# Kernel optimization log

Measured on AMD Instinct MI355X. Metric: run time of the kernel, lower is better.

Reference implementation:

```python
import jax, jax.numpy as jnp
import numpy as np

N_NODES = 100000
N_EDGES = 1600000
IN_CH = 128
OUT_CH = 32
HEADS = 2
NEG_SLOPE = 0.2  # GATv2Conv default negative_slope


def setup_inputs() -> dict:
    key = jax.random.key(0)
    ks = jax.random.split(key, 6)
    x = jax.random.normal(ks[0], (N_NODES, IN_CH), dtype=jnp.float32)
    edge_index = jax.random.randint(ks[1], (2, N_EDGES), 0, N_NODES, dtype=jnp.int64)
    s_in = 1.0 / np.sqrt(IN_CH)
    Wl = jax.random.normal(ks[2], (IN_CH, HEADS * OUT_CH), dtype=jnp.float32) * s_in  # lin_l weight
    Wr = jax.random.normal(ks[3], (IN_CH, HEADS * OUT_CH), dtype=jnp.float32) * s_in  # lin_r weight
    bl = jnp.zeros((HEADS * OUT_CH,), dtype=jnp.float32)
    br = jnp.zeros((HEADS * OUT_CH,), dtype=jnp.float32)
    att = jax.random.normal(ks[4], (HEADS, OUT_CH), dtype=jnp.float32) * (1.0 / np.sqrt(OUT_CH))
    bias = jnp.zeros((OUT_CH,), dtype=jnp.float32)  # output bias (concat=False -> size out_channels)
    return {"x": x, "Wl": Wl, "bl": bl, "Wr": Wr, "br": br, "att": att, "bias": bias,
            "edge_index": edge_index}


def _gatv2_layer(x, Wl, bl, Wr, br, att, bias, edge_index):
    N = x.shape[0]
    H, C = att.shape
    # add self loops (GATv2Conv default add_self_loops=True)
    loops = jnp.arange(N, dtype=edge_index.dtype)
    src = jnp.concatenate([edge_index[0], loops])  # [E+N] message sources j
    dst = jnp.concatenate([edge_index[1], loops])  # [E+N] message targets i
    # per-node linear transforms (share_weights=False)
    xl = (x @ Wl + bl).reshape(N, H, C)
    xr = (x @ Wr + br).reshape(N, H, C)
    # GATv2 dynamic attention: a^T LeakyReLU(xl[j] + xr[i])
    h = xl[src] + xr[dst]                                   # [E, H, C]
    e = jnp.einsum('ehc,hc->eh', jax.nn.leaky_relu(h, NEG_SLOPE), att)  # [E, H]
    # segment softmax over incoming edges of each target node
    m = jax.ops.segment_max(e, dst, num_segments=N)         # [N, H]
    a = jnp.exp(e - m[dst])
    denom = jax.ops.segment_sum(a, dst, num_segments=N)     # [N, H]
    alpha = a / (denom[dst] + 1e-16)                        # [E, H]
    # weighted scatter-add of source messages
    out = jax.ops.segment_sum(alpha[:, :, None] * xl[src], dst, num_segments=N)  # [N, H, C]
    out = out.mean(axis=1) + bias                           # concat=False -> head mean
    return jax.nn.silu(out)                                 # activation='silu'


def reference(x, Wl, bl, Wr, br, att, bias, edge_index):
    return _gatv2_layer(x, Wl, bl, Wr, br, att, bias, edge_index)
```

## Files before the change

### kernel.cpp

```cpp
#include <hip/hip_runtime.h>
#include <math.h>

#define BSH 9
#define BMASK ((1 << BSH) - 1)
#define CAP 12288
#define ACH 2048

typedef unsigned int uint;
typedef __attribute__((ext_vector_type(8))) short bf16x8;
typedef __attribute__((ext_vector_type(4))) float f32x4;
typedef __attribute__((ext_vector_type(2))) float f32x2;

static __device__ __forceinline__ unsigned short f2bf(float f) {
    uint u = __float_as_uint(f);
    return (unsigned short)((u + 0x7fffu + ((u >> 16) & 1u)) >> 16);
}

static __device__ __forceinline__ bf16x8 pack8(f32x4 a, f32x4 b) {
    uint p0, p1, p2, p3;
    asm("v_cvt_pk_bf16_f32 %0, %1, %2" : "=v"(p0) : "v"(a.x), "v"(a.y));
    asm("v_cvt_pk_bf16_f32 %0, %1, %2" : "=v"(p1) : "v"(a.z), "v"(a.w));
    asm("v_cvt_pk_bf16_f32 %0, %1, %2" : "=v"(p2) : "v"(b.x), "v"(b.y));
    asm("v_cvt_pk_bf16_f32 %0, %1, %2" : "=v"(p3) : "v"(b.z), "v"(b.w));
    uint4 u = make_uint4(p0, p1, p2, p3);
    return *(bf16x8*)&u;
}

static __device__ __forceinline__ f32x2 dec2(uint u) {
    f32x2 r;
    r.x = __uint_as_float(u << 16);
    r.y = __uint_as_float(u & 0xffff0000u);
    return r;
}

static __device__ __forceinline__ f32x2 abs2(f32x2 h) {
    f32x2 r;
    r.x = __uint_as_float(__float_as_uint(h.x) & 0x7fffffffu);
    r.y = __uint_as_float(__float_as_uint(h.y) & 0x7fffffffu);
    return r;
}

static __device__ __forceinline__ float qsum(float p) {
    p += __uint_as_float(__builtin_amdgcn_mov_dpp(__float_as_uint(p), 0xB1, 0xF, 0xF, true));
    p += __uint_as_float(__builtin_amdgcn_mov_dpp(__float_as_uint(p), 0x4E, 0xF, 0xF, true));
    return p;
}

__global__ __launch_bounds__(256) void k_prep(const float* __restrict__ Wl,
                                              const float* __restrict__ Wr,
                                              unsigned short* __restrict__ Wt) {
    int si = blockIdx.x * 256 + threadIdx.x;
    int lo = si & 15;
    int hi = (si >> 4) & 3;
    int j  = (si >> 6) & 7;
    int ks = si >> 9;
    int n  = j * 16 + lo;
    int kb = ks * 32 + hi * 8;
    const float* Wp = (n < 64) ? (Wl + n) : (Wr + (n - 64));
    unsigned short v[8];
#pragma unroll
    for (int m = 0; m < 8; ++m)
        v[m] = f2bf(Wp[(size_t)(kb + m) * 64]);
    uint4 pk;
    pk.x = (uint)v[0] | ((uint)v[1] << 16);
    pk.y = (uint)v[2] | ((uint)v[3] << 16);
    pk.z = (uint)v[4] | ((uint)v[5] << 16);
    pk.w = (uint)v[6] | ((uint)v[7] << 16);
    *(uint4*)(Wt + (size_t)si * 8) = pk;
}

static __device__ __forceinline__ void gemm_body(
        const float* __restrict__ x, const unsigned short* __restrict__ Wt,
        const float* __restrict__ bl, const float* __restrict__ br,
        unsigned short* __restrict__ xlh, unsigned short* __restrict__ xrh, int N, int bid)
{
    const int t = threadIdx.x;
    const int base = bid * 128;
    const int w = t >> 6;
    const int lo = t & 15;
    const int hi = (t & 63) >> 4;
    int row0 = base + w * 32 + lo;
    int row1 = row0 + 16;
    const f32x4* x40 = (const f32x4*)x + (size_t)(row0 < N ? row0 : N - 1) * 32;
    const f32x4* x41 = (const f32x4*)x + (size_t)(row1 < N ? row1 : N - 1) * 32;
    const bf16x8* Wf = (const bf16x8*)Wt;

    f32x4 acc[2][8];
#pragma unroll
    for (int f = 0; f < 2; ++f)
#pragma unroll
        for (int j = 0; j < 8; ++j)
            acc[f][j] = (f32x4){0.f, 0.f, 0.f, 0.f};

#pragma unroll
    for (int ks = 0; ks < 4; ++ks) {
        int f4 = ks * 8 + hi * 2;
        int sbase = ks * 512 + hi * 16 + lo;
        bf16x8 av[2], bv[8];
        av[0] = pack8(__builtin_nontemporal_load(x40 + f4),
                      __builtin_nontemporal_load(x40 + f4 + 1));
        av[1] = pack8(__builtin_nontemporal_load(x41 + f4),
                      __builtin_nontemporal_load(x41 + f4 + 1));
#pragma unroll
        for (int j = 0; j < 8; ++j)
            bv[j] = Wf[sbase + j * 64];
#pragma unroll
        for (int f = 0; f < 2; ++f)
#pragma unroll
            for (int j = 0; j < 8; ++j)
                acc[f][j] = __builtin_amdgcn_mfma_f32_16x16x32_bf16(av[f], bv[j], acc[f][j], 0, 0, 0);
    }

#pragma unroll
    for (int f = 0; f < 2; ++f) {
        int rbase = base + w * 32 + f * 16 + hi * 4;
#pragma unroll
        for (int j = 0; j < 8; ++j) {
            int nn = j * 16 + lo;
            float bvv = (j < 4) ? bl[nn] : br[nn - 64];
            unsigned short* dst = (j < 4) ? (xlh + nn) : (xrh + (nn - 64));
#pragma unroll
            for (int q = 0; q < 4; ++q)
                if (rbase + q < N) dst[(size_t)(rbase + q) * 64] = f2bf(acc[f][j][q] + bvv);
        }
    }
}

static __device__ __forceinline__ void scatA_body(
        const int* __restrict__ ei, int* __restrict__ bcur,
        unsigned* __restrict__ pairs, int E, int T, int NB, int bid)
{
    __shared__ int h[256];
    __shared__ int basem[256];
    int b0 = bid * ACH;
    int cnt = min(ACH, T - b0);
    h[threadIdx.x] = 0;
    __syncthreads();
    for (int i = threadIdx.x; i < cnt; i += 256) {
        int t = b0 + i;
        int d = (t < E) ? ei[E + t] : (t - E);
        atomicAdd(&h[d >> BSH], 1);
    }
    __syncthreads();
    if (threadIdx.x < NB) {
        int c = h[threadIdx.x];
        basem[threadIdx.x] = c ? (threadIdx.x * CAP + atomicAdd(&bcur[threadIdx.x], c)) : 0;
    }
    __syncthreads();
    h[threadIdx.x] = 0;
    __syncthreads();
    for (int i = threadIdx.x; i < cnt; i += 256) {
        int t = b0 + i;
        int s, d;
        if (t < E) { s = ei[t]; d = ei[E + t]; } else { s = t - E; d = s; }
        int b = d >> BSH;
        int idx = atomicAdd(&h[b], 1);
        pairs[basem[b] + idx] = ((unsigned)s << BSH) | (unsigned)(d & BMASK);
    }
}

__global__ __launch_bounds__(256) void k_gs(const float* __restrict__ x,
        const unsigned short* __restrict__ Wt,
        const float* __restrict__ bl, const float* __restrict__ br,
        unsigned short* __restrict__ xlh, unsigned short* __restrict__ xrh, int N,
        const int* __restrict__ ei, int* __restrict__ bcur,
        unsigned* __restrict__ pairs, int E, int T, int NB, int GB)
{
    if ((int)blockIdx.x < GB)
        gemm_body(x, Wt, bl, br, xlh, xrh, N, blockIdx.x);
    else
        scatA_body(ei, bcur, pairs, E, T, NB, blockIdx.x - GB);
}

__global__ __launch_bounds__(512) void k_scatB(const unsigned* __restrict__ pairs,
                                               const int* __restrict__ bcur,
                                               int* __restrict__ src_s, int2* __restrict__ rowrng, int N) {
    __shared__ int cnt[512];
    __shared__ int sm[512];
    __shared__ int lofs[512];
    int b = blockIdx.x;
    int beg = b * CAP, end = beg + bcur[b];
    int nbase = b << BSH;
    cnt[threadIdx.x] = 0;
    __syncthreads();
    for (int i = beg + threadIdx.x; i < end; i += 512)
        atomicAdd(&cnt[pairs[i] & BMASK], 1);
    __syncthreads();
    int v = cnt[threadIdx.x];
    sm[threadIdx.x] = v;
    __syncthreads();
    int acc = v;
    for (int off = 1; off < 512; off <<= 1) {
        int t = (threadIdx.x >= off) ? sm[threadIdx.x - off] : 0;
        __syncthreads();
        acc += t;
        sm[threadIdx.x] = acc;
        __syncthreads();
    }
    int excl = acc - v;
    lofs[threadIdx.x] = excl;
    int n = nbase + threadIdx.x;
    if (n < N) rowrng[n] = make_int2(beg + excl, beg + excl + v);
    cnt[threadIdx.x] = 0;
    __syncthreads();
    for (int i = beg + threadIdx.x; i < end; i += 512) {
        unsigned p = pairs[i];
        int dl = p & BMASK;
        int idx = atomicAdd(&cnt[dl], 1);
        src_s[beg + lofs[dl] + idx] = p >> BSH;
    }
}

__global__ __launch_bounds__(256) void k_fused(const int2* __restrict__ rowrng,
        const int* __restrict__ src_s, const unsigned short* __restrict__ xlh,
        const unsigned short* __restrict__ xrh, const float* __restrict__ att,
        const float* __restrict__ bias, float* __restrict__ out, int N)
{
    int n = blockIdx.x * 32 + (threadIdx.x >> 3);
    int j = threadIdx.x & 7;
    if (n >= N) return;
    const uint4* xl4 = (const uint4*)xlh + j;
    f32x2 xr2[4], a06[4], a04[4];
    {
        uint4 u = ((const uint4*)xrh)[(size_t)n * 8 + j];
        xr2[0] = dec2(u.x); xr2[1] = dec2(u.y);
        xr2[2] = dec2(u.z); xr2[3] = dec2(u.w);
        float4 c = ((const float4*)att)[j * 2];
        float4 d = ((const float4*)att)[j * 2 + 1];
        a06[0] = (f32x2){0.6f * c.x, 0.6f * c.y}; a06[1] = (f32x2){0.6f * c.z, 0.6f * c.w};
        a06[2] = (f32x2){0.6f * d.x, 0.6f * d.y}; a06[3] = (f32x2){0.6f * d.z, 0.6f * d.w};
        a04[0] = (f32x2){0.4f * c.x, 0.4f * c.y}; a04[1] = (f32x2){0.4f * c.z, 0.4f * c.w};
        a04[2] = (f32x2){0.4f * d.x, 0.4f * d.y}; a04[3] = (f32x2){0.4f * d.z, 0.4f * d.w};
    }
    int2 rr = rowrng[n];
    float ssum = 0.f;
    f32x2 acc2[4] = {(f32x2){0.f,0.f}, (f32x2){0.f,0.f}, (f32x2){0.f,0.f}, (f32x2){0.f,0.f}};

#define EDGE_BODY(u)                                                      \
    {                                                                     \
        f32x2 v0 = dec2((u).x), v1 = dec2((u).y), v2 = dec2((u).z), v3 = dec2((u).w); \
        f32x2 h0 = v0 + xr2[0], h1 = v1 + xr2[1], h2 = v2 + xr2[2], h3 = v3 + xr2[3]; \
        f32x2 pa = h0 * a06[0]; pa += h1 * a06[1]; pa += h2 * a06[2]; pa += h3 * a06[3]; \
        pa += abs2(h0) * a04[0]; pa += abs2(h1) * a04[1];                 \
        pa += abs2(h2) * a04[2]; pa += abs2(h3) * a04[3];                 \
        float p = pa.x + pa.y;                                            \
        p = qsum(p);                                                      \
        float wq = __expf(p);                                             \
        ssum += wq;                                                       \
        f32x2 ws = (f32x2){wq, wq};                                       \
        acc2[0] += ws * v0; acc2[1] += ws * v1;                           \
        acc2[2] += ws * v2; acc2[3] += ws * v3;                           \
    }

    int i = rr.x;
    for (; i + 8 <= rr.y; i += 8) {
        uint4 u[8];
#pragma unroll
        for (int q = 0; q < 8; ++q)
            u[q] = xl4[((uint)src_s[i + q] << 3)];
#pragma unroll
        for (int q = 0; q < 8; ++q)
            EDGE_BODY(u[q]);
    }
    if (i + 4 <= rr.y) {
        uint4 u[4];
#pragma unroll
        for (int q = 0; q < 4; ++q)
            u[q] = xl4[((uint)src_s[i + q] << 3)];
#pragma unroll
        for (int q = 0; q < 4; ++q)
            EDGE_BODY(u[q]);
        i += 4;
    }
    for (; i < rr.y; ++i) {
        uint4 u0 = xl4[((uint)src_s[i] << 3)];
        EDGE_BODY(u0);
    }
#undef EDGE_BODY

    float inv = 1.f / ssum;
    float o[8];
#pragma unroll
    for (int q = 0; q < 4; ++q) {
        float vx = acc2[q].x * inv, vy = acc2[q].y * inv;
        o[2 * q]     = (vx + __shfl_xor(vx, 4)) * 0.5f;
        o[2 * q + 1] = (vy + __shfl_xor(vy, 4)) * 0.5f;
    }
    if (j < 4) {
        float4 b0 = ((const float4*)bias)[j * 2];
        float4 b1 = ((const float4*)bias)[j * 2 + 1];
        float4 r0, r1;
        r0.x = o[0] + b0.x; r0.y = o[1] + b0.y; r0.z = o[2] + b0.z; r0.w = o[3] + b0.w;
        r1.x = o[4] + b1.x; r1.y = o[5] + b1.y; r1.z = o[6] + b1.z; r1.w = o[7] + b1.w;
        r0.x = r0.x / (1.f + __expf(-r0.x));
        r0.y = r0.y / (1.f + __expf(-r0.y));
        r0.z = r0.z / (1.f + __expf(-r0.z));
        r0.w = r0.w / (1.f + __expf(-r0.w));
        r1.x = r1.x / (1.f + __expf(-r1.x));
        r1.y = r1.y / (1.f + __expf(-r1.y));
        r1.z = r1.z / (1.f + __expf(-r1.z));
        r1.w = r1.w / (1.f + __expf(-r1.w));
        ((float4*)out)[(size_t)n * 8 + j * 2] = r0;
        ((float4*)out)[(size_t)n * 8 + j * 2 + 1] = r1;
    }
}

extern "C" void kernel_launch(void* const* d_in, const int* in_sizes, int n_in,
                              void* d_out, int out_size, void* d_ws, size_t ws_size,
                              hipStream_t stream) {
    const float* x    = (const float*)d_in[0];
    const float* Wl   = (const float*)d_in[1];
    const float* bl   = (const float*)d_in[2];
    const float* Wr   = (const float*)d_in[3];
    const float* br   = (const float*)d_in[4];
    const float* att  = (const float*)d_in[5];
    const float* bias = (const float*)d_in[6];
    const int*   ei   = (const int*)d_in[7];
    float* out = (float*)d_out;

    const int N = in_sizes[0] / 128;
    const int E = in_sizes[7] / 2;
    const int T = E + N;
    const int NB = (N + (1 << BSH) - 1) >> BSH;

    char* p = (char*)d_ws;
    auto take = [&](size_t bytes) {
        char* r = p;
        p += (bytes + 255) & ~(size_t)255;
        return r;
    };
    unsigned short* xlh = (unsigned short*)take((size_t)N * 64 * 2);
    unsigned short* xrh = (unsigned short*)take((size_t)N * 64 * 2);
    unsigned* pairs  = (unsigned*)take((size_t)NB * CAP * 4);
    int*      src_s  = (int*)take((size_t)NB * CAP * 4);
    int2*     rowrng = (int2*)take((size_t)N * 8);
    int*      bcur   = (int*)take((size_t)NB * 4);
    unsigned short* Wt = (unsigned short*)take((size_t)128 * 128 * 2);

    const int GB = (N + 127) / 128;
    const int SB = (T + ACH - 1) / ACH;
    hipMemsetAsync(bcur, 0, (size_t)NB * 4, stream);
    k_prep <<<8,             256, 0, stream>>>(Wl, Wr, Wt);
    k_gs   <<<GB + SB,       256, 0, stream>>>(x, Wt, bl, br, xlh, xrh, N,
                                               ei, bcur, pairs, E, T, NB, GB);
    k_scatB<<<NB,            512, 0, stream>>>(pairs, bcur, src_s, rowrng, N);
    k_fused<<<(N + 31) / 32, 256, 0, stream>>>(rowrng, src_s, xlh, xrh, att, bias, out, N);
}
```

Baseline: 118.6 us.

## Interleave scatter and GEMM blocks, coalesce bf16 projection stores, enlarge scatter chunks

The GEMM epilogue now writes xl/xr rows as packed bf16 pairs in an interleaved column layout instead of scattered 2-byte stores. The fused kernel's attention, bias and output indexing are remapped to match that layout. Scatter blocks are spread evenly among the GEMM blocks in the combined launch rather than placed after them, so the two kinds of work run concurrently. The scatter chunk size grows fourfold and nontemporal loads are dropped. Larger chunks mean fewer scatter blocks, each with longer serial work.

New measurement: 110.4 us. 6.9% less time.

```diff
diff --git a/kernel.cpp b/kernel.cpp
--- a/kernel.cpp
+++ b/kernel.cpp
@@ -4,7 +4,7 @@
 #define BSH 9
 #define BMASK ((1 << BSH) - 1)
 #define CAP 12288
-#define ACH 2048
+#define ACH 8192
 
 typedef unsigned int uint;
 typedef __attribute__((ext_vector_type(8))) short bf16x8;
@@ -24,6 +24,12 @@
     asm("v_cvt_pk_bf16_f32 %0, %1, %2" : "=v"(p3) : "v"(b.z), "v"(b.w));
     uint4 u = make_uint4(p0, p1, p2, p3);
     return *(bf16x8*)&u;
+}
+
+static __device__ __forceinline__ uint pk2(float a, float b) {
+    uint d;
+    asm("v_cvt_pk_bf16_f32 %0, %1, %2" : "=v"(d) : "v"(a), "v"(b));
+    return d;
 }
 
 static __device__ __forceinline__ f32x2 dec2(uint u) {
@@ -97,10 +103,8 @@
         int f4 = ks * 8 + hi * 2;
         int sbase = ks * 512 + hi * 16 + lo;
         bf16x8 av[2], bv[8];
-        av[0] = pack8(__builtin_nontemporal_load(x40 + f4),
-                      __builtin_nontemporal_load(x40 + f4 + 1));
-        av[1] = pack8(__builtin_nontemporal_load(x41 + f4),
-                      __builtin_nontemporal_load(x41 + f4 + 1));
+        av[0] = pack8(x40[f4], x40[f4 + 1]);
+        av[1] = pack8(x41[f4], x41[f4 + 1]);
 #pragma unroll
         for (int j = 0; j < 8; ++j)
             bv[j] = Wf[sbase + j * 64];
@@ -111,17 +115,24 @@
                 acc[f][j] = __builtin_amdgcn_mfma_f32_16x16x32_bf16(av[f], bv[j], acc[f][j], 0, 0, 0);
     }
 
+    float blv[4], brv[4];
+#pragma unroll
+    for (int t2 = 0; t2 < 4; ++t2) {
+        blv[t2] = bl[t2 * 16 + lo];
+        brv[t2] = br[t2 * 16 + lo];
+    }
 #pragma unroll
     for (int f = 0; f < 2; ++f) {
-        int rbase = base + w * 32 + f * 16 + hi * 4;
-#pragma unroll
-        for (int j = 0; j < 8; ++j) {
-            int nn = j * 16 + lo;
-            float bvv = (j < 4) ? bl[nn] : br[nn - 64];
-            unsigned short* dst = (j < 4) ? (xlh + nn) : (xrh + (nn - 64));
-#pragma unroll
-            for (int q = 0; q < 4; ++q)
-                if (rbase + q < N) dst[(size_t)(rbase + q) * 64] = f2bf(acc[f][j][q] + bvv);
+#pragma unroll
+        for (int q = 0; q < 4; ++q) {
+            int row = base + w * 32 + f * 16 + hi * 4 + q;
+            if (row < N) {
+                size_t rb = (size_t)row * 64;
+                *(uint*)(xlh + rb + 2 * lo)      = pk2(acc[f][0][q] + blv[0], acc[f][1][q] + blv[1]);
+                *(uint*)(xlh + rb + 32 + 2 * lo) = pk2(acc[f][2][q] + blv[2], acc[f][3][q] + blv[3]);
+                *(uint*)(xrh + rb + 2 * lo)      = pk2(acc[f][4][q] + brv[0], acc[f][5][q] + brv[1]);
+                *(uint*)(xrh + rb + 32 + 2 * lo) = pk2(acc[f][6][q] + brv[2], acc[f][7][q] + brv[3]);
+            }
         }
     }
 }
@@ -164,12 +175,15 @@
         const float* __restrict__ bl, const float* __restrict__ br,
         unsigned short* __restrict__ xlh, unsigned short* __restrict__ xrh, int N,
         const int* __restrict__ ei, int* __restrict__ bcur,
-        unsigned* __restrict__ pairs, int E, int T, int NB, int GB)
+        unsigned* __restrict__ pairs, int E, int T, int NB, int SB, int R)
 {
-    if ((int)blockIdx.x < GB)
-        gemm_body(x, Wt, bl, br, xlh, xrh, N, blockIdx.x);
+    int bid = blockIdx.x;
+    int sbef = (int)(((long long)bid * SB) / R);
+    int snow = (int)(((long long)(bid + 1) * SB) / R);
+    if (snow > sbef)
+        scatA_body(ei, bcur, pairs, E, T, NB, sbef);
     else
-        scatA_body(ei, bcur, pairs, E, T, NB, blockIdx.x - GB);
+        gemm_body(x, Wt, bl, br, xlh, xrh, N, bid - sbef);
 }
 
 __global__ __launch_bounds__(512) void k_scatB(const unsigned* __restrict__ pairs,
@@ -217,20 +231,22 @@
         const float* __restrict__ bias, float* __restrict__ out, int N)
 {
     int n = blockIdx.x * 32 + (threadIdx.x >> 3);
-    int j = threadIdx.x & 7;
+    int jf = threadIdx.x & 7;
     if (n >= N) return;
-    const uint4* xl4 = (const uint4*)xlh + j;
+    int hsel = jf >> 2, l4 = jf & 3;
+    const uint4* xl4 = (const uint4*)xlh + jf;
     f32x2 xr2[4], a06[4], a04[4];
     {
-        uint4 u = ((const uint4*)xrh)[(size_t)n * 8 + j];
+        uint4 u = ((const uint4*)xrh)[(size_t)n * 8 + jf];
         xr2[0] = dec2(u.x); xr2[1] = dec2(u.y);
         xr2[2] = dec2(u.z); xr2[3] = dec2(u.w);
-        float4 c = ((const float4*)att)[j * 2];
-        float4 d = ((const float4*)att)[j * 2 + 1];
-        a06[0] = (f32x2){0.6f * c.x, 0.6f * c.y}; a06[1] = (f32x2){0.6f * c.z, 0.6f * c.w};
-        a06[2] = (f32x2){0.6f * d.x, 0.6f * d.y}; a06[3] = (f32x2){0.6f * d.z, 0.6f * d.w};
-        a04[0] = (f32x2){0.4f * c.x, 0.4f * c.y}; a04[1] = (f32x2){0.4f * c.z, 0.4f * c.w};
-        a04[2] = (f32x2){0.4f * d.x, 0.4f * d.y}; a04[3] = (f32x2){0.4f * d.z, 0.4f * d.w};
+        int cb = hsel * 32 + 4 * l4;
+#pragma unroll
+        for (int k = 0; k < 4; ++k) {
+            float c0 = att[cb + k], c1 = att[cb + 16 + k];
+            a06[k] = (f32x2){0.6f * c0, 0.6f * c1};
+            a04[k] = (f32x2){0.4f * c0, 0.4f * c1};
+        }
     }
     int2 rr = rowrng[n];
     float ssum = 0.f;
@@ -286,12 +302,12 @@
         o[2 * q]     = (vx + __shfl_xor(vx, 4)) * 0.5f;
         o[2 * q + 1] = (vy + __shfl_xor(vy, 4)) * 0.5f;
     }
-    if (j < 4) {
-        float4 b0 = ((const float4*)bias)[j * 2];
-        float4 b1 = ((const float4*)bias)[j * 2 + 1];
+    if (jf < 4) {
+        float4 b0 = ((const float4*)bias)[l4];
+        float4 b1 = *(const float4*)(bias + 16 + 4 * l4);
         float4 r0, r1;
-        r0.x = o[0] + b0.x; r0.y = o[1] + b0.y; r0.z = o[2] + b0.z; r0.w = o[3] + b0.w;
-        r1.x = o[4] + b1.x; r1.y = o[5] + b1.y; r1.z = o[6] + b1.z; r1.w = o[7] + b1.w;
+        r0.x = o[0] + b0.x; r0.y = o[2] + b0.y; r0.z = o[4] + b0.z; r0.w = o[6] + b0.w;
+        r1.x = o[1] + b1.x; r1.y = o[3] + b1.y; r1.z = o[5] + b1.z; r1.w = o[7] + b1.w;
         r0.x = r0.x / (1.f + __expf(-r0.x));
         r0.y = r0.y / (1.f + __expf(-r0.y));
         r0.z = r0.z / (1.f + __expf(-r0.z));
@@ -300,8 +316,8 @@
         r1.y = r1.y / (1.f + __expf(-r1.y));
         r1.z = r1.z / (1.f + __expf(-r1.z));
         r1.w = r1.w / (1.f + __expf(-r1.w));
-        ((float4*)out)[(size_t)n * 8 + j * 2] = r0;
-        ((float4*)out)[(size_t)n * 8 + j * 2 + 1] = r1;
+        ((float4*)out)[(size_t)n * 8 + l4]     = r0;
+        ((float4*)out)[(size_t)n * 8 + 4 + l4] = r1;
     }
 }
 
@@ -339,10 +355,11 @@
 
     const int GB = (N + 127) / 128;
     const int SB = (T + ACH - 1) / ACH;
+    const int R  = GB + SB;
     hipMemsetAsync(bcur, 0, (size_t)NB * 4, stream);
     k_prep <<<8,             256, 0, stream>>>(Wl, Wr, Wt);
-    k_gs   <<<GB + SB,       256, 0, stream>>>(x, Wt, bl, br, xlh, xrh, N,
-                                               ei, bcur, pairs, E, T, NB, GB);
+    k_gs   <<<R,             256, 0, stream>>>(x, Wt, bl, br, xlh, xrh, N,
+                                               ei, bcur, pairs, E, T, NB, SB, R);
     k_scatB<<<NB,            512, 0, stream>>>(pairs, bcur, src_s, rowrng, N);
     k_fused<<<(N + 31) / 32, 256, 0, stream>>>(rowrng, src_s, xlh, xrh, att, bias, out, N);
 }
```
